# Performance work log

Measured on AMD Instinct MI355X. Metric: run time of the kernel, lower is better.

Reference implementation:

```python
import jax, jax.numpy as jnp
from jax import lax
import numpy as np

B, N, D = 32, 8192, 256
EPS = 1e-06        # module eps
NUM = 1e-06        # numerator epsilon in tan_theta
BN_EPS = 1e-05     # torch BatchNorm1d default
SLOPE = 0.2        # LeakyReLU negative_slope

REG = jnp.array([[-1, -1, -1, 0, 0, 0, 1, 1, 1],
                 [-1,  0,  1, -1, 0, 1, -1, 0, 1]], dtype=jnp.float32)  # [2,9]


def conv1d(x, w, b):
    # x: [B,C,N], w: [O,C,3], pad=1 -> [B,O,N]
    y = lax.conv_general_dilated(x, w, (1,), [(1, 1)],
                                 dimension_numbers=('NCH', 'OIH', 'NCH'))
    return y + b[None, :, None]


def batchnorm(x, gamma, beta):
    # training-mode BatchNorm1d over (B, N) per channel, biased variance
    m = x.mean(axis=(0, 2), keepdims=True)
    v = ((x - m) ** 2).mean(axis=(0, 2), keepdims=True)
    return gamma[None, :, None] * (x - m) * lax.rsqrt(v + BN_EPS) + beta[None, :, None]


def setup_inputs() -> dict:
    key = jax.random.key(0)
    ks = jax.random.split(key, 12)
    s = 0.05
    return {
        'pts':      jax.random.normal(ks[0], (B, 2, N), jnp.float32),
        'feats':    jax.random.normal(ks[1], (B, D, N), jnp.float32),
        'rot_w':    jax.random.normal(ks[2], (4, D, 3), jnp.float32) * s,
        'rot_b':    jax.random.normal(ks[3], (4,), jnp.float32) * s,
        'trans_w':  jax.random.normal(ks[4], (2, D, 3), jnp.float32) * s,
        'trans_b':  jax.random.normal(ks[5], (2,), jnp.float32) * s,
        'pos_w':    jax.random.normal(ks[6], (2, 20, 3), jnp.float32) * s,
        'pos_b':    jax.random.normal(ks[7], (2,), jnp.float32) * s,
        'pos_g':    jnp.ones((2,), jnp.float32),
        'pos_beta': jnp.zeros((2,), jnp.float32),
        'ori_w':    jax.random.normal(ks[8], (2, 2, 3), jnp.float32) * s,
        'ori_b':    jax.random.normal(ks[9], (2,), jnp.float32) * s,
        'ori_g':    jnp.ones((2,), jnp.float32),
        'ori_beta': jnp.zeros((2,), jnp.float32),
    }


def compute_offset(feats, rot_w, rot_b, trans_w, trans_b):
    b, _, n = feats.shape
    tm = conv1d(feats, rot_w, rot_b)                       # [B,4,N]
    tm = tm.transpose(0, 2, 1).reshape(b, n, 2, 2)         # per-point 2x2
    transformed = jnp.einsum('bnij,jk->bnik', tm, REG)     # [B,N,2,9]
    offset = transformed - REG                             # broadcast [2,9]
    # transpose(1,2).reshape(B,N,18).permute -> interleaved (x0,y0,x1,y1,...)
    offset = offset.transpose(0, 1, 3, 2).reshape(b, n, 18).transpose(0, 2, 1)  # [B,18,N]
    translation = conv1d(feats, trans_w, trans_b)          # [B,2,N]
    # even channels += tx, odd channels += ty
    off = offset.reshape(b, 9, 2, n) + translation[:, None, :, :]
    return off.reshape(b, 18, n)


def reference(pts, feats, rot_w, rot_b, trans_w, trans_b,
              pos_w, pos_b, pos_g, pos_beta,
              ori_w, ori_b, ori_g, ori_beta):
    b, _, n = pts.shape
    offset = compute_offset(feats, rot_w, rot_b, trans_w, trans_b)  # [B,18,N]

    # geo_position branch
    x = jnp.concatenate([pts, offset], axis=1)             # [B,20,N]
    x = conv1d(x, pos_w, pos_b)                            # [B,2,N]
    x = batchnorm(x, pos_g, pos_beta)
    x = jnp.where(x >= 0, x, SLOPE * x)                    # LeakyReLU(0.2)

    # geo_orientation branch
    off_x = offset[:, 0::2, :]                             # [B,9,N]
    off_y = offset[:, 1::2, :]
    rad = jnp.arctan((off_y + NUM) / (off_x + EPS))        # [B,9,N]
    main_rad = rad.max(axis=1)                             # [B,N]
    c, s = jnp.cos(main_rad), jnp.sin(main_rad)
    # rotation[b,n] = [[cos, sin], [-sin, cos]]
    rot = jnp.stack([jnp.stack([c, s], -1), jnp.stack([-s, c], -1)], -2)  # [B,N,2,2]
    x = jnp.einsum('bxn,bnxy->byn', x, rot)                # rotate 2-d coords
    x = conv1d(x, ori_w, ori_b)
    x = batchnorm(x, ori_g, ori_beta)
    return x
```

## Files before the change

kernel.cpp:

```cpp
#include <hip/hip_runtime.h>
#include <math.h>

#define NPTS 8192
#define DCH  256
#define BB   32
#define TOTPT (BB * NPTS)

#define T_OFF    0
#define X1_OFF   (BB * 6 * NPTS)
#define COS_OFF  (X1_OFF + BB * 2 * NPTS)
#define SIN_OFF  (COS_OFF + TOTPT)
#define X5_OFF   (SIN_OFF + TOTPT)
#define STATS_OFF (X5_OFF + BB * 2 * NPTS)

__global__ __launch_bounds__(256) void convA(
    const float* __restrict__ feats,
    const float* __restrict__ rot_w, const float* __restrict__ rot_b,
    const float* __restrict__ trans_w, const float* __restrict__ trans_b,
    float* __restrict__ T)
{
    const int blk  = blockIdx.x;
    const int b    = blk >> 5;
    const int n0   = (blk & 31) << 8;
    const int wave = threadIdx.x >> 6;
    const int lane = threadIdx.x & 63;
    const int p    = n0 + (lane << 2);

    const float* fb = feats + (size_t)b * DCH * NPTS;

    float acc[6][4];
#pragma unroll
    for (int o = 0; o < 6; ++o)
#pragma unroll
        for (int j = 0; j < 4; ++j) acc[o][j] = 0.0f;

    const int c0 = __builtin_amdgcn_readfirstlane(wave << 6);

    const float lmask = (p > 0) ? 1.0f : 0.0f;
    const int   lidx  = (p > 0) ? (p - 1) : 0;
    const float rmask = (p + 4 < NPTS) ? 1.0f : 0.0f;
    const int   ridx  = (p + 4 < NPTS) ? (p + 4) : 0;

    const float* fr = fb + (size_t)c0 * NPTS;

#pragma unroll 4
    for (int cc = 0; cc < 64; ++cc) {
        const int c = c0 + cc;
        const float4 v = *(const float4*)(fr + p);
        const float fl = fr[lidx] * lmask;
        const float fd = fr[ridx] * rmask;
        const float f[6] = { fl, v.x, v.y, v.z, v.w, fd };
#pragma unroll
        for (int o = 0; o < 6; ++o) {
            const float* wp = (o < 4) ? (rot_w + ((size_t)o * DCH + c) * 3)
                                      : (trans_w + ((size_t)(o - 4) * DCH + c) * 3);
            const float w0 = wp[0], w1 = wp[1], w2 = wp[2];
#pragma unroll
            for (int j = 0; j < 4; ++j)
                acc[o][j] += w0 * f[j] + w1 * f[j + 1] + w2 * f[j + 2];
        }
        fr += NPTS;
    }

    __shared__ float red[3][64][25];
    if (wave >= 1) {
#pragma unroll
        for (int o = 0; o < 6; ++o)
#pragma unroll
            for (int j = 0; j < 4; ++j)
                red[wave - 1][lane][o * 4 + j] = acc[o][j];
    }
    __syncthreads();
    if (wave == 0) {
#pragma unroll
        for (int q = 0; q < 3; ++q)
#pragma unroll
            for (int o = 0; o < 6; ++o)
#pragma unroll
                for (int j = 0; j < 4; ++j)
                    acc[o][j] += red[q][lane][o * 4 + j];
#pragma unroll
        for (int o = 0; o < 6; ++o) {
            const float bias = (o < 4) ? rot_b[o] : trans_b[o - 4];
            float4 outv = make_float4(acc[o][0] + bias, acc[o][1] + bias,
                                      acc[o][2] + bias, acc[o][3] + bias);
            *(float4*)(T + ((size_t)b * 6 + o) * NPTS + p) = outv;
        }
    }
}

__device__ __forceinline__ void block_reduce_atomic4(float v0, float v1,
                                                     float v2, float v3,
                                                     float* dst)
{
#pragma unroll
    for (int off = 32; off > 0; off >>= 1) {
        v0 += __shfl_down(v0, off, 64);
        v1 += __shfl_down(v1, off, 64);
        v2 += __shfl_down(v2, off, 64);
        v3 += __shfl_down(v3, off, 64);
    }
    __shared__ float red[4][4];
    const int wave = threadIdx.x >> 6, lane = threadIdx.x & 63;
    if (lane == 0) {
        red[wave][0] = v0; red[wave][1] = v1; red[wave][2] = v2; red[wave][3] = v3;
    }
    __syncthreads();
    if (threadIdx.x == 0) {
        float a0 = 0, a1 = 0, a2 = 0, a3 = 0;
#pragma unroll
        for (int w = 0; w < 4; ++w) {
            a0 += red[w][0]; a1 += red[w][1]; a2 += red[w][2]; a3 += red[w][3];
        }
        atomicAdd(dst + 0, a0); atomicAdd(dst + 1, a1);
        atomicAdd(dst + 2, a2); atomicAdd(dst + 3, a3);
    }
}

__global__ __launch_bounds__(256) void kernB(
    const float* __restrict__ pts, const float* __restrict__ T,
    const float* __restrict__ pos_w, const float* __restrict__ pos_b,
    float* __restrict__ x1, float* __restrict__ cosA, float* __restrict__ sinA,
    float* __restrict__ stats)
{
    const int g = blockIdx.x * 256 + threadIdx.x;
    const int b = g >> 13;
    const int n = g & (NPTS - 1);

    float xs0 = pos_b[0], xs1 = pos_b[1];
    float ctr[18];
    float mz = -INFINITY;

#pragma unroll
    for (int m3 = 0; m3 < 3; ++m3) {
        const int m   = n + m3 - 1;
        const float msk = (m >= 0 && m < NPTS) ? 1.0f : 0.0f;
        const int mc  = (m < 0) ? 0 : ((m >= NPTS) ? NPTS - 1 : m);
        float t[6];
#pragma unroll
        for (int o = 0; o < 6; ++o)
            t[o] = T[((size_t)b * 6 + o) * NPTS + mc];
        float cat[20];
        cat[0] = pts[((size_t)b * 2 + 0) * NPTS + mc];
        cat[1] = pts[((size_t)b * 2 + 1) * NPTS + mc];
        const float o0 = t[0] - 1.0f, o1 = t[1];
        const float o2 = t[2], o3 = t[3] - 1.0f;
        const float tr0 = t[4], tr1 = t[5];
#pragma unroll
        for (int k = 0; k < 9; ++k) {
            const float R0 = (float)(k / 3 - 1);
            const float R1 = (float)(k % 3 - 1);
            cat[2 + 2 * k]     = o0 * R0 + o1 * R1 + tr0;
            cat[2 + 2 * k + 1] = o2 * R0 + o3 * R1 + tr1;
        }
        if (m3 == 1) {
#pragma unroll
            for (int cc = 0; cc < 18; ++cc) ctr[cc] = cat[2 + cc];
        }
        float p0 = 0.0f, p1 = 0.0f;
#pragma unroll
        for (int c = 0; c < 20; ++c) {
            p0 += pos_w[0 * 60 + c * 3 + m3] * cat[c];
            p1 += pos_w[1 * 60 + c * 3 + m3] * cat[c];
        }
        xs0 += msk * p0;
        xs1 += msk * p1;
    }

#pragma unroll
    for (int k = 0; k < 9; ++k) {
        const float ox = ctr[2 * k], oy = ctr[2 * k + 1];
        const float z = (oy + 1e-6f) / (ox + 1e-6f);
        mz = fmaxf(mz, z);
    }
    const float mr = atanf(mz);
    float sv, cv;
    sincosf(mr, &sv, &cv);

    x1[((size_t)b * 2 + 0) * NPTS + n] = xs0;
    x1[((size_t)b * 2 + 1) * NPTS + n] = xs1;
    cosA[g] = cv;
    sinA[g] = sv;

    block_reduce_atomic4(xs0, xs1, xs0 * xs0, xs1 * xs1, stats);
}

__global__ __launch_bounds__(256) void kernD(
    const float* __restrict__ x1,
    const float* __restrict__ cosA, const float* __restrict__ sinA,
    const float* __restrict__ pos_g, const float* __restrict__ pos_beta,
    const float* __restrict__ ori_w, const float* __restrict__ ori_b,
    float* __restrict__ stats, float* __restrict__ x5)
{
    const int g = blockIdx.x * 256 + threadIdx.x;
    const int b = g >> 13;
    const int n = g & (NPTS - 1);

    const float cntInv = 1.0f / (float)TOTPT;
    const float m0 = stats[0] * cntInv, m1 = stats[1] * cntInv;
    const float var0 = stats[2] * cntInv - m0 * m0;
    const float var1 = stats[3] * cntInv - m1 * m1;
    const float i0 = rsqrtf(var0 + 1e-5f), i1 = rsqrtf(var1 + 1e-5f);
    const float g0 = pos_g[0], g1 = pos_g[1];
    const float be0 = pos_beta[0], be1 = pos_beta[1];

    float x4a[3], x4b[3];
#pragma unroll
    for (int m3 = 0; m3 < 3; ++m3) {
        const int m   = n + m3 - 1;
        const float msk = (m >= 0 && m < NPTS) ? 1.0f : 0.0f;
        const int mc  = (m < 0) ? 0 : ((m >= NPTS) ? NPTS - 1 : m);
        float y0 = x1[((size_t)b * 2 + 0) * NPTS + mc];
        float y1 = x1[((size_t)b * 2 + 1) * NPTS + mc];
        y0 = g0 * (y0 - m0) * i0 + be0;
        y1 = g1 * (y1 - m1) * i1 + be1;
        y0 = (y0 >= 0.0f) ? y0 : 0.2f * y0;
        y1 = (y1 >= 0.0f) ? y1 : 0.2f * y1;
        const float cv = cosA[(b << 13) + mc];
        const float sv = sinA[(b << 13) + mc];
        x4a[m3] = (y0 * cv - y1 * sv) * msk;
        x4b[m3] = (y0 * sv + y1 * cv) * msk;
    }

    float z0 = ori_b[0], z1 = ori_b[1];
#pragma unroll
    for (int k = 0; k < 3; ++k) {
        z0 += ori_w[0 * 6 + 0 * 3 + k] * x4a[k] + ori_w[0 * 6 + 1 * 3 + k] * x4b[k];
        z1 += ori_w[1 * 6 + 0 * 3 + k] * x4a[k] + ori_w[1 * 6 + 1 * 3 + k] * x4b[k];
    }
    x5[((size_t)b * 2 + 0) * NPTS + n] = z0;
    x5[((size_t)b * 2 + 1) * NPTS + n] = z1;

    block_reduce_atomic4(z0, z1, z0 * z0, z1 * z1, stats + 4);
}

__global__ __launch_bounds__(256) void kernE(
    const float* __restrict__ x5, const float* __restrict__ stats,
    const float* __restrict__ ori_g, const float* __restrict__ ori_beta,
    float* __restrict__ out)
{
    const int g = blockIdx.x * 256 + threadIdx.x;
    const int o = (g >> 13) & 1;
    const float cntInv = 1.0f / (float)TOTPT;
    const float m  = stats[4 + o] * cntInv;
    const float vv = stats[6 + o] * cntInv - m * m;
    const float inv = rsqrtf(vv + 1e-5f);
    out[g] = ori_g[o] * (x5[g] - m) * inv + ori_beta[o];
}

extern "C" void kernel_launch(void* const* d_in, const int* in_sizes, int n_in,
                              void* d_out, int out_size, void* d_ws, size_t ws_size,
                              hipStream_t stream)
{
    const float* pts      = (const float*)d_in[0];
    const float* feats    = (const float*)d_in[1];
    const float* rot_w    = (const float*)d_in[2];
    const float* rot_b    = (const float*)d_in[3];
    const float* trans_w  = (const float*)d_in[4];
    const float* trans_b  = (const float*)d_in[5];
    const float* pos_w    = (const float*)d_in[6];
    const float* pos_b    = (const float*)d_in[7];
    const float* pos_g    = (const float*)d_in[8];
    const float* pos_beta = (const float*)d_in[9];
    const float* ori_w    = (const float*)d_in[10];
    const float* ori_b    = (const float*)d_in[11];
    const float* ori_g    = (const float*)d_in[12];
    const float* ori_beta = (const float*)d_in[13];

    float* ws   = (float*)d_ws;
    float* T    = ws + T_OFF;
    float* x1   = ws + X1_OFF;
    float* cosA = ws + COS_OFF;
    float* sinA = ws + SIN_OFF;
    float* x5   = ws + X5_OFF;
    float* stats = ws + STATS_OFF;

    hipMemsetAsync(stats, 0, 8 * sizeof(float), stream);

    convA<<<1024, 256, 0, stream>>>(feats, rot_w, rot_b, trans_w, trans_b, T);
    kernB<<<1024, 256, 0, stream>>>(pts, T, pos_w, pos_b, x1, cosA, sinA, stats);
    kernD<<<1024, 256, 0, stream>>>(x1, cosA, sinA, pos_g, pos_beta,
                                    ori_w, ori_b, stats, x5);
    kernE<<<2048, 256, 0, stream>>>(x5, stats, ori_g, ori_beta, (float*)d_out);
}
```

Before: 499.7 us.

## Fuse feature conv into offset/position kernel and spread BN stat atomics

Merges the feature convolution kernel with the offset/position-conv kernel. The six-channel conv output now stays in shared memory instead of going through a global intermediate, and the halo points at each tile edge are recomputed by a per-channel cross-lane reduction. Batch-norm statistics atomics are spread over 16 slots per stage, and the consumers sum those slots, to reduce atomic contention. This removes a launch and the round trip of the intermediate buffer, at the cost of extra halo work and more shared memory in the fused kernel.

```diff
diff --git a/kernel.cpp b/kernel.cpp
--- a/kernel.cpp
+++ b/kernel.cpp
@@ -6,27 +6,61 @@
 #define BB   32
 #define TOTPT (BB * NPTS)
 
-#define T_OFF    0
-#define X1_OFF   (BB * 6 * NPTS)
-#define COS_OFF  (X1_OFF + BB * 2 * NPTS)
-#define SIN_OFF  (COS_OFF + TOTPT)
-#define X5_OFF   (SIN_OFF + TOTPT)
+#define X1_OFF    0
+#define COS_OFF   (X1_OFF + BB * 2 * NPTS)
+#define SIN_OFF   (COS_OFF + TOTPT)
+#define X5_OFF    (SIN_OFF + TOTPT)
 #define STATS_OFF (X5_OFF + BB * 2 * NPTS)
 
-__global__ __launch_bounds__(256) void convA(
-    const float* __restrict__ feats,
+__device__ __forceinline__ void block_reduce_atomic4(float v0, float v1,
+                                                     float v2, float v3,
+                                                     float* dst)
+{
+#pragma unroll
+    for (int off = 32; off > 0; off >>= 1) {
+        v0 += __shfl_down(v0, off, 64);
+        v1 += __shfl_down(v1, off, 64);
+        v2 += __shfl_down(v2, off, 64);
+        v3 += __shfl_down(v3, off, 64);
+    }
+    __shared__ float red[4][4];
+    const int wave = threadIdx.x >> 6, lane = threadIdx.x & 63;
+    if (lane == 0) {
+        red[wave][0] = v0; red[wave][1] = v1; red[wave][2] = v2; red[wave][3] = v3;
+    }
+    __syncthreads();
+    if (threadIdx.x == 0) {
+        float a0 = 0, a1 = 0, a2 = 0, a3 = 0;
+#pragma unroll
+        for (int w = 0; w < 4; ++w) {
+            a0 += red[w][0]; a1 += red[w][1]; a2 += red[w][2]; a3 += red[w][3];
+        }
+        atomicAdd(dst + 0, a0); atomicAdd(dst + 1, a1);
+        atomicAdd(dst + 2, a2); atomicAdd(dst + 3, a3);
+    }
+}
+
+__global__ __launch_bounds__(256) void kernAB(
+    const float* __restrict__ pts, const float* __restrict__ feats,
     const float* __restrict__ rot_w, const float* __restrict__ rot_b,
     const float* __restrict__ trans_w, const float* __restrict__ trans_b,
-    float* __restrict__ T)
+    const float* __restrict__ pos_w, const float* __restrict__ pos_b,
+    float* __restrict__ x1, float* __restrict__ cosA, float* __restrict__ sinA,
+    float* __restrict__ stats)
 {
     const int blk  = blockIdx.x;
     const int b    = blk >> 5;
     const int n0   = (blk & 31) << 8;
-    const int wave = threadIdx.x >> 6;
-    const int lane = threadIdx.x & 63;
+    const int tid  = threadIdx.x;
+    const int wave = tid >> 6;
+    const int lane = tid & 63;
     const int p    = n0 + (lane << 2);
 
     const float* fb = feats + (size_t)b * DCH * NPTS;
+
+    __shared__ float red[3][64][25];
+    __shared__ float hw4[4][12];
+    __shared__ float Tsh[6][260];
 
     float acc[6][4];
 #pragma unroll
@@ -62,7 +96,30 @@
         fr += NPTS;
     }
 
-    __shared__ float red[3][64][25];
+    float hh[12];
+    {
+        const float* fc = fb + (size_t)tid * NPTS;
+        const int iA = (n0 >= 2) ? (n0 - 2) : 0;
+        const int iB = (n0 >= 1) ? (n0 - 1) : 0;
+        const float a0 = fc[iA], a1 = fc[iB], a2 = fc[n0];
+        const int jB = (n0 + 256 <= NPTS - 1) ? (n0 + 256) : (NPTS - 1);
+        const int jC = (n0 + 257 <= NPTS - 1) ? (n0 + 257) : (NPTS - 1);
+        const float b0 = fc[n0 + 255], b1 = fc[jB], b2 = fc[jC];
+#pragma unroll
+        for (int o = 0; o < 6; ++o) {
+            const float* wp = (o < 4) ? (rot_w + ((size_t)o * DCH + tid) * 3)
+                                      : (trans_w + ((size_t)(o - 4) * DCH + tid) * 3);
+            const float w0 = wp[0], w1 = wp[1], w2 = wp[2];
+            hh[o]     = w0 * a0 + w1 * a1 + w2 * a2;
+            hh[6 + o] = w0 * b0 + w1 * b1 + w2 * b2;
+        }
+    }
+#pragma unroll
+    for (int off = 32; off > 0; off >>= 1)
+#pragma unroll
+        for (int j = 0; j < 12; ++j)
+            hh[j] += __shfl_down(hh[j], off, 64);
+
     if (wave >= 1) {
 #pragma unroll
         for (int o = 0; o < 6; ++o)
@@ -70,7 +127,12 @@
             for (int j = 0; j < 4; ++j)
                 red[wave - 1][lane][o * 4 + j] = acc[o][j];
     }
+    if (lane == 0) {
+#pragma unroll
+        for (int j = 0; j < 12; ++j) hw4[wave][j] = hh[j];
+    }
     __syncthreads();
+
     if (wave == 0) {
 #pragma unroll
         for (int q = 0; q < 3; ++q)
@@ -82,53 +144,28 @@
 #pragma unroll
         for (int o = 0; o < 6; ++o) {
             const float bias = (o < 4) ? rot_b[o] : trans_b[o - 4];
-            float4 outv = make_float4(acc[o][0] + bias, acc[o][1] + bias,
-                                      acc[o][2] + bias, acc[o][3] + bias);
-            *(float4*)(T + ((size_t)b * 6 + o) * NPTS + p) = outv;
-        }
-    }
-}
-
-__device__ __forceinline__ void block_reduce_atomic4(float v0, float v1,
-                                                     float v2, float v3,
-                                                     float* dst)
-{
-#pragma unroll
-    for (int off = 32; off > 0; off >>= 1) {
-        v0 += __shfl_down(v0, off, 64);
-        v1 += __shfl_down(v1, off, 64);
-        v2 += __shfl_down(v2, off, 64);
-        v3 += __shfl_down(v3, off, 64);
-    }
-    __shared__ float red[4][4];
-    const int wave = threadIdx.x >> 6, lane = threadIdx.x & 63;
-    if (lane == 0) {
-        red[wave][0] = v0; red[wave][1] = v1; red[wave][2] = v2; red[wave][3] = v3;
+#pragma unroll
+            for (int j = 0; j < 4; ++j)
+                Tsh[o][1 + (lane << 2) + j] = acc[o][j] + bias;
+        }
+    }
+    if (tid < 12) {
+        const int o = tid % 6, side = tid / 6;
+        float v = hw4[0][tid] + hw4[1][tid] + hw4[2][tid] + hw4[3][tid];
+        v += (o < 4) ? rot_b[o] : trans_b[o - 4];
+        Tsh[o][side ? 257 : 0] = v;
     }
     __syncthreads();
-    if (threadIdx.x == 0) {
-        float a0 = 0, a1 = 0, a2 = 0, a3 = 0;
-#pragma unroll
-        for (int w = 0; w < 4; ++w) {
-            a0 += red[w][0]; a1 += red[w][1]; a2 += red[w][2]; a3 += red[w][3];
-        }
-        atomicAdd(dst + 0, a0); atomicAdd(dst + 1, a1);
-        atomicAdd(dst + 2, a2); atomicAdd(dst + 3, a3);
-    }
-}
-
-__global__ __launch_bounds__(256) void kernB(
-    const float* __restrict__ pts, const float* __restrict__ T,
-    const float* __restrict__ pos_w, const float* __restrict__ pos_b,
-    float* __restrict__ x1, float* __restrict__ cosA, float* __restrict__ sinA,
-    float* __restrict__ stats)
-{
-    const int g = blockIdx.x * 256 + threadIdx.x;
-    const int b = g >> 13;
-    const int n = g & (NPTS - 1);
+
+    const int n = n0 + tid;
+    float tm[6][3];
+#pragma unroll
+    for (int o = 0; o < 6; ++o)
+#pragma unroll
+        for (int k = 0; k < 3; ++k)
+            tm[o][k] = Tsh[o][tid + k];
 
     float xs0 = pos_b[0], xs1 = pos_b[1];
-    float ctr[18];
     float mz = -INFINITY;
 
 #pragma unroll
@@ -136,53 +173,47 @@
         const int m   = n + m3 - 1;
         const float msk = (m >= 0 && m < NPTS) ? 1.0f : 0.0f;
         const int mc  = (m < 0) ? 0 : ((m >= NPTS) ? NPTS - 1 : m);
-        float t[6];
-#pragma unroll
-        for (int o = 0; o < 6; ++o)
-            t[o] = T[((size_t)b * 6 + o) * NPTS + mc];
-        float cat[20];
-        cat[0] = pts[((size_t)b * 2 + 0) * NPTS + mc];
-        cat[1] = pts[((size_t)b * 2 + 1) * NPTS + mc];
-        const float o0 = t[0] - 1.0f, o1 = t[1];
-        const float o2 = t[2], o3 = t[3] - 1.0f;
-        const float tr0 = t[4], tr1 = t[5];
+
+        const float pa = pts[((size_t)b * 2 + 0) * NPTS + mc];
+        const float pb = pts[((size_t)b * 2 + 1) * NPTS + mc];
+
+        const float o0 = tm[0][m3] - 1.0f, o1 = tm[1][m3];
+        const float o2 = tm[2][m3],        o3 = tm[3][m3] - 1.0f;
+        const float tr0 = tm[4][m3],       tr1 = tm[5][m3];
+
+        float p0 = pos_w[0 * 60 + 0 * 3 + m3] * pa + pos_w[0 * 60 + 1 * 3 + m3] * pb;
+        float p1 = pos_w[1 * 60 + 0 * 3 + m3] * pa + pos_w[1 * 60 + 1 * 3 + m3] * pb;
 #pragma unroll
         for (int k = 0; k < 9; ++k) {
             const float R0 = (float)(k / 3 - 1);
             const float R1 = (float)(k % 3 - 1);
-            cat[2 + 2 * k]     = o0 * R0 + o1 * R1 + tr0;
-            cat[2 + 2 * k + 1] = o2 * R0 + o3 * R1 + tr1;
-        }
-        if (m3 == 1) {
-#pragma unroll
-            for (int cc = 0; cc < 18; ++cc) ctr[cc] = cat[2 + cc];
-        }
-        float p0 = 0.0f, p1 = 0.0f;
-#pragma unroll
-        for (int c = 0; c < 20; ++c) {
-            p0 += pos_w[0 * 60 + c * 3 + m3] * cat[c];
-            p1 += pos_w[1 * 60 + c * 3 + m3] * cat[c];
+            const float cx = o0 * R0 + o1 * R1 + tr0;
+            const float cy = o2 * R0 + o3 * R1 + tr1;
+            p0 += pos_w[0 * 60 + (2 + 2 * k) * 3 + m3] * cx
+                + pos_w[0 * 60 + (3 + 2 * k) * 3 + m3] * cy;
+            p1 += pos_w[1 * 60 + (2 + 2 * k) * 3 + m3] * cx
+                + pos_w[1 * 60 + (3 + 2 * k) * 3 + m3] * cy;
+            if (m3 == 1) {
+                const float z = (cy + 1e-6f) / (cx + 1e-6f);
+                mz = fmaxf(mz, z);
+            }
         }
         xs0 += msk * p0;
         xs1 += msk * p1;
     }
 
-#pragma unroll
-    for (int k = 0; k < 9; ++k) {
-        const float ox = ctr[2 * k], oy = ctr[2 * k + 1];
-        const float z = (oy + 1e-6f) / (ox + 1e-6f);
-        mz = fmaxf(mz, z);
-    }
     const float mr = atanf(mz);
     float sv, cv;
     sincosf(mr, &sv, &cv);
 
+    const int g = (b << 13) + n;
     x1[((size_t)b * 2 + 0) * NPTS + n] = xs0;
     x1[((size_t)b * 2 + 1) * NPTS + n] = xs1;
     cosA[g] = cv;
     sinA[g] = sv;
 
-    block_reduce_atomic4(xs0, xs1, xs0 * xs0, xs1 * xs1, stats);
+    block_reduce_atomic4(xs0, xs1, xs0 * xs0, xs1 * xs1,
+                         stats + ((blk & 15) << 2));
 }
 
 __global__ __launch_bounds__(256) void kernD(
@@ -192,14 +223,20 @@
     const float* __restrict__ ori_w, const float* __restrict__ ori_b,
     float* __restrict__ stats, float* __restrict__ x5)
 {
-    const int g = blockIdx.x * 256 + threadIdx.x;
-    const int b = g >> 13;
-    const int n = g & (NPTS - 1);
-
+    const int gg = blockIdx.x * 256 + threadIdx.x;
+    const int b = gg >> 13;
+    const int n = gg & (NPTS - 1);
+
+    float s0 = 0, s1 = 0, s2 = 0, s3 = 0;
+#pragma unroll
+    for (int q = 0; q < 16; ++q) {
+        s0 += stats[q * 4 + 0]; s1 += stats[q * 4 + 1];
+        s2 += stats[q * 4 + 2]; s3 += stats[q * 4 + 3];
+    }
     const float cntInv = 1.0f / (float)TOTPT;
-    const float m0 = stats[0] * cntInv, m1 = stats[1] * cntInv;
-    const float var0 = stats[2] * cntInv - m0 * m0;
-    const float var1 = stats[3] * cntInv - m1 * m1;
+    const float m0 = s0 * cntInv, m1 = s1 * cntInv;
+    const float var0 = s2 * cntInv - m0 * m0;
+    const float var1 = s3 * cntInv - m1 * m1;
     const float i0 = rsqrtf(var0 + 1e-5f), i1 = rsqrtf(var1 + 1e-5f);
     const float g0 = pos_g[0], g1 = pos_g[1];
     const float be0 = pos_beta[0], be1 = pos_beta[1];
@@ -231,7 +268,8 @@
     x5[((size_t)b * 2 + 0) * NPTS + n] = z0;
     x5[((size_t)b * 2 + 1) * NPTS + n] = z1;
 
-    block_reduce_atomic4(z0, z1, z0 * z0, z1 * z1, stats + 4);
+    block_reduce_atomic4(z0, z1, z0 * z0, z1 * z1,
+                         stats + 64 + ((blockIdx.x & 15) << 2));
 }
 
 __global__ __launch_bounds__(256) void kernE(
@@ -239,13 +277,19 @@
     const float* __restrict__ ori_g, const float* __restrict__ ori_beta,
     float* __restrict__ out)
 {
-    const int g = blockIdx.x * 256 + threadIdx.x;
-    const int o = (g >> 13) & 1;
+    const int gg = blockIdx.x * 256 + threadIdx.x;
+    const int o = (gg >> 13) & 1;
+    float sm = 0, sq = 0;
+#pragma unroll
+    for (int q = 0; q < 16; ++q) {
+        sm += stats[64 + q * 4 + o];
+        sq += stats[64 + q * 4 + 2 + o];
+    }
     const float cntInv = 1.0f / (float)TOTPT;
-    const float m  = stats[4 + o] * cntInv;
-    const float vv = stats[6 + o] * cntInv - m * m;
+    const float m  = sm * cntInv;
+    const float vv = sq * cntInv - m * m;
     const float inv = rsqrtf(vv + 1e-5f);
-    out[g] = ori_g[o] * (x5[g] - m) * inv + ori_beta[o];
+    out[gg] = ori_g[o] * (x5[gg] - m) * inv + ori_beta[o];
 }
 
 extern "C" void kernel_launch(void* const* d_in, const int* in_sizes, int n_in,
@@ -267,18 +311,17 @@
     const float* ori_g    = (const float*)d_in[12];
     const float* ori_beta = (const float*)d_in[13];
 
-    float* ws   = (float*)d_ws;
-    float* T    = ws + T_OFF;
-    float* x1   = ws + X1_OFF;
-    float* cosA = ws + COS_OFF;
-    float* sinA = ws + SIN_OFF;
-    float* x5   = ws + X5_OFF;
+    float* ws    = (float*)d_ws;
+    float* x1    = ws + X1_OFF;
+    float* cosA  = ws + COS_OFF;
+    float* sinA  = ws + SIN_OFF;
+    float* x5    = ws + X5_OFF;
     float* stats = ws + STATS_OFF;
 
-    hipMemsetAsync(stats, 0, 8 * sizeof(float), stream);
-
-    convA<<<1024, 256, 0, stream>>>(feats, rot_w, rot_b, trans_w, trans_b, T);
-    kernB<<<1024, 256, 0, stream>>>(pts, T, pos_w, pos_b, x1, cosA, sinA, stats);
+    hipMemsetAsync(stats, 0, 128 * sizeof(float), stream);
+
+    kernAB<<<1024, 256, 0, stream>>>(pts, feats, rot_w, rot_b, trans_w, trans_b,
+                                     pos_w, pos_b, x1, cosA, sinA, stats);
     kernD<<<1024, 256, 0, stream>>>(x1, cosA, sinA, pos_g, pos_beta,
                                     ori_w, ori_b, stats, x5);
     kernE<<<2048, 256, 0, stream>>>(x5, stats, ori_g, ori_beta, (float*)d_out);
```

After: 499.2 us (median of 2 runs). Within noise of the previous version (-0.1%).
